# Performance work log

Measured on AMD Instinct MI355X. Metric: run time of the kernel, lower is better.

## Reference

```python
import jax, jax.numpy as jnp
import numpy as np

E = 8          # moe_expert_count
CAPACITY = 1024  # per-expert capacity C = S / E (capacity factor 1)


def _top1_gate(features, wg):
    """Top-1 gate with capacity, returning combine_weights [S,E,C],
    dispatch_mask [S,E,C], and load-balancing aux loss (standard Switch/BASE-style gate
    matching the (l_aux, combine_weights, dispatch_mask) interface used by BaseLayer)."""
    S, M = features.shape
    logits = features @ wg                      # [S, E]
    gates = jax.nn.softmax(logits, axis=-1)     # [S, E]
    idx = jnp.argmax(gates, axis=-1)            # [S] expert assignment
    mask1 = jax.nn.one_hot(idx, E, dtype=features.dtype)  # [S, E]
    # position of each token inside its expert's buffer (0-based, order of arrival)
    locations = jnp.cumsum(mask1, axis=0) - mask1          # [S, E]
    loc = jnp.sum(locations * mask1, axis=1).astype(jnp.int32)  # [S]
    keep = (loc < CAPACITY).astype(features.dtype)          # drop overflow tokens
    mask1 = mask1 * keep[:, None]
    gate_s = jnp.sum(gates * mask1, axis=1)                 # [S] gate prob of kept tokens
    loc_oh = jax.nn.one_hot(loc, CAPACITY, dtype=features.dtype)  # [S, C]
    combine = gate_s[:, None, None] * mask1[:, :, None] * loc_oh[:, None, :]  # [S,E,C]
    dispatch = (combine > 0).astype(features.dtype)
    # load-balance aux loss: E * sum(mean_prob_e * frac_tokens_e)
    me = jnp.mean(gates, axis=0)
    ce = jnp.mean(mask1, axis=0)
    l_aux = jnp.sum(me * ce) * E
    return l_aux, combine, dispatch


def setup_inputs() -> dict:
    key = jax.random.key(0)
    k0, k1, k2, k3 = jax.random.split(key, 4)
    B, T, M, H = 4, 2048, 512, 1024
    return {
        "hidden_states": jax.random.normal(k0, (B, T, M), dtype=jnp.float32),
        "wg": jax.random.normal(k1, (M, E), dtype=jnp.float32) * 0.02,
        "w1": jax.random.normal(k2, (E, M, H), dtype=jnp.float32) * 0.02,
        "b1": jnp.zeros((E, H), dtype=jnp.float32),
        "w2": jax.random.normal(k3, (E, H, M), dtype=jnp.float32) * 0.02,
        "b2": jnp.zeros((E, M), dtype=jnp.float32),
    }


def reference(hidden_states, wg, w1, b1, w2, b2):
    B, T, M = hidden_states.shape
    feats = hidden_states.reshape(-1, M)            # [S, M]
    l_aux, combine, dispatch = _top1_gate(feats, wg)
    # dense one-hot dispatch matmul: (E*C, S) @ (S, M) -> [E, C, M]
    dispatched = jnp.einsum('sec,sm->ecm', dispatch, feats)
    # per-expert FFN (BaseSublayer: Linear -> ReLU -> Linear)
    h = jax.nn.relu(jnp.einsum('ecm,emh->ech', dispatched, w1) + b1[:, None, :])
    expert_out = jnp.einsum('ech,ehn->ecn', h, w2) + b2[:, None, :]  # [E, C, M]
    # dense combine matmul: (S, E*C) @ (E*C, M) -> [S, M]
    combined = jnp.einsum('sec,ecn->sn', combine, expert_out)
    return combined.reshape(B, T, -1), l_aux
```

## Files before the change

### kernel.cpp

```cpp
#include <hip/hip_runtime.h>

#define S_TOK 8192
#define M_DIM 512
#define E_NUM 8
#define CAP   1024
#define H_DIM 1024
#define NGATE_BLK (S_TOK / 4)

typedef __attribute__((ext_vector_type(8))) short bf16x8;
typedef __attribute__((ext_vector_type(16))) float f32x16;

__device__ static inline unsigned short f2bf(float f) {
    unsigned int u = __float_as_uint(f);
    unsigned int r = (u + 0x7fffu + ((u >> 16) & 1u)) >> 16;
    return (unsigned short)r;
}

__device__ static inline void async_copy16(const void* g, void* l) {
    __builtin_amdgcn_global_load_lds(
        (const __attribute__((address_space(1))) void*)g,
        (__attribute__((address_space(3))) void*)l, 16, 0, 0);
}

__global__ __launch_bounds__(256) void prep_kernel(
    const float* __restrict__ feats, const float* __restrict__ wg,
    int* __restrict__ idx, float* __restrict__ gate_top,
    float* __restrict__ gates_psum, unsigned short* __restrict__ xb,
    const float* __restrict__ w1, unsigned short* __restrict__ w1t,
    const float* __restrict__ w2, unsigned short* __restrict__ w2t)
{
    __shared__ float gsh[4][8];
    __shared__ float tile[64][65];

    if (blockIdx.x < NGATE_BLK) {
        const int wave = threadIdx.x >> 6;
        const int lane = threadIdx.x & 63;
        const int s = blockIdx.x * 4 + wave;

        const float* xrow = feats + (size_t)s * M_DIM;
        const int m0 = lane * 8;

        const float4 va = *(const float4*)(xrow + m0);
        const float4 vb = *(const float4*)(xrow + m0 + 4);
        float xv[8] = {va.x, va.y, va.z, va.w, vb.x, vb.y, vb.z, vb.w};

        {
            bf16x8 o;
#pragma unroll
            for (int j = 0; j < 8; ++j) o[j] = (short)f2bf(xv[j]);
            *(bf16x8*)(xb + (size_t)s * M_DIM + m0) = o;
            if (blockIdx.x == 0 && wave == 0) {
                bf16x8 z = (bf16x8){0,0,0,0,0,0,0,0};
                *(bf16x8*)(xb + (size_t)S_TOK * M_DIM + m0) = z;
            }
        }

        float p[8];
#pragma unroll
        for (int e = 0; e < 8; ++e) p[e] = 0.f;
#pragma unroll
        for (int j = 0; j < 8; ++j) {
            const float4 wa = *(const float4*)(wg + (m0 + j) * 8);
            const float4 wb2 = *(const float4*)(wg + (m0 + j) * 8 + 4);
            const float x = xv[j];
            p[0] += x * wa.x;  p[1] += x * wa.y;  p[2] += x * wa.z;  p[3] += x * wa.w;
            p[4] += x * wb2.x; p[5] += x * wb2.y; p[6] += x * wb2.z; p[7] += x * wb2.w;
        }
#pragma unroll
        for (int e = 0; e < 8; ++e) {
            float v = p[e];
#pragma unroll
            for (int off = 1; off < 64; off <<= 1) v += __shfl_xor(v, off, 64);
            p[e] = v;
        }
        if (lane == 0) {
            float mx = p[0];
#pragma unroll
            for (int e = 1; e < 8; ++e) mx = fmaxf(mx, p[e]);
            float ex[8], sum = 0.f;
#pragma unroll
            for (int e = 0; e < 8; ++e) { ex[e] = expf(p[e] - mx); sum += ex[e]; }
            const float inv = 1.0f / sum;
            int best = 0; float bl = p[0];
#pragma unroll
            for (int e = 1; e < 8; ++e) { if (p[e] > bl) { bl = p[e]; best = e; } }
#pragma unroll
            for (int e = 0; e < 8; ++e) gsh[wave][e] = ex[e] * inv;
            idx[s] = best;
            gate_top[s] = ex[best] * inv;
        }
        __syncthreads();
        if (threadIdx.x < 8) {
            const int e = threadIdx.x;
            gates_psum[blockIdx.x * 8 + e] =
                gsh[0][e] + gsh[1][e] + gsh[2][e] + gsh[3][e];
        }
    } else {
        int b = blockIdx.x - NGATE_BLK;
        const float* src; unsigned short* dst;
        int e, k0, n0, K, N;
        if (b < 1024) {
            e = b >> 7; const int rem = b & 127;
            k0 = (rem >> 4) * 64; n0 = (rem & 15) * 64;
            K = 512; N = 1024; src = w1; dst = w1t;
        } else {
            b -= 1024;
            e = b >> 7; const int rem = b & 127;
            k0 = (rem >> 3) * 64; n0 = (rem & 7) * 64;
            K = 1024; N = 512; src = w2; dst = w2t;
        }
        const int t = threadIdx.x;
        const int r = t >> 4, c4 = (t & 15) * 4;
#pragma unroll
        for (int i = 0; i < 4; ++i) {
            const int row = r + i * 16;
            const float4 v = *(const float4*)(src + ((size_t)e * K + k0 + row) * N + n0 + c4);
            tile[row][c4 + 0] = v.x; tile[row][c4 + 1] = v.y;
            tile[row][c4 + 2] = v.z; tile[row][c4 + 3] = v.w;
        }
        __syncthreads();
#pragma unroll
        for (int i = 0; i < 4; ++i) {
            const int row = r + i * 16;
            ushort4 o;
            o.x = f2bf(tile[c4 + 0][row]); o.y = f2bf(tile[c4 + 1][row]);
            o.z = f2bf(tile[c4 + 2][row]); o.w = f2bf(tile[c4 + 3][row]);
            *(ushort4*)(dst + ((size_t)e * N + n0 + row) * K + k0 + c4) = o;
        }
    }
}

__global__ __launch_bounds__(256) void scan_kernel(
    const int* __restrict__ idx, const float* __restrict__ gate_top,
    const float* __restrict__ gates_psum,
    float* __restrict__ gate_final, int* __restrict__ token_list,
    int* __restrict__ kept, float* __restrict__ out,
    int* __restrict__ dropped)
{
    __shared__ int   cnts[256][9];
    __shared__ float wpart[4][8];
    __shared__ int   totals[8];
    __shared__ float gfbuf[8192];
    __shared__ int   dropctr;

    const int t = threadIdx.x;
    const int wv = t >> 6, ln = t & 63;
    const int base = t * 32;

    if (t == 0) dropctr = 0;

    int4   vi[8];
    float4 vg[8];
#pragma unroll
    for (int i = 0; i < 8; ++i) vi[i] = ((const int4*)(idx + base))[i];
#pragma unroll
    for (int i = 0; i < 8; ++i) vg[i] = ((const float4*)(gate_top + base))[i];

    {
        const int4 s4 = make_int4(S_TOK, S_TOK, S_TOK, S_TOK);
#pragma unroll
        for (int i = 0; i < 8; ++i) ((int4*)token_list)[t + 256 * i] = s4;
    }

    int c[8];
#pragma unroll
    for (int e = 0; e < 8; ++e) c[e] = 0;
#pragma unroll
    for (int i = 0; i < 8; ++i) {
#pragma unroll
        for (int e = 0; e < 8; ++e)
            c[e] += (vi[i].x == e) + (vi[i].y == e) + (vi[i].z == e) + (vi[i].w == e);
    }

    float g[8];
#pragma unroll
    for (int e = 0; e < 8; ++e) g[e] = 0.f;
#pragma unroll
    for (int i = 0; i < NGATE_BLK / 256; ++i) {
        const float* gp = gates_psum + (size_t)(t + 256 * i) * 8;
        const float4 a = *(const float4*)gp;
        const float4 b = *(const float4*)(gp + 4);
        g[0] += a.x; g[1] += a.y; g[2] += a.z; g[3] += a.w;
        g[4] += b.x; g[5] += b.y; g[6] += b.z; g[7] += b.w;
    }
#pragma unroll
    for (int e = 0; e < 8; ++e) cnts[t][e] = c[e];
#pragma unroll
    for (int e = 0; e < 8; ++e) {
        float v = g[e];
#pragma unroll
        for (int off = 1; off < 64; off <<= 1) v += __shfl_xor(v, off, 64);
        if (ln == 0) wpart[wv][e] = v;
    }
    __syncthreads();

#pragma unroll
    for (int ee = 0; ee < 2; ++ee) {
        const int e = wv * 2 + ee;
        int off = 0;
#pragma unroll
        for (int seg = 0; seg < 4; ++seg) {
            const int r = seg * 64 + ln;
            const int v = cnts[r][e];
            int incl = v;
#pragma unroll
            for (int d = 1; d < 64; d <<= 1) {
                const int nn = __shfl_up(incl, d, 64);
                if (ln >= d) incl += nn;
            }
            cnts[r][e] = incl - v + off;
            off += __shfl(incl, 63, 64);
        }
        if (ln == 0) {
            totals[e] = off;
            kept[e] = off < CAP ? off : CAP;
        }
    }
    __syncthreads();

    if (t == 0) {
        float l = 0.f;
        for (int e = 0; e < 8; ++e) {
            const float ms = wpart[0][e] + wpart[1][e] + wpart[2][e] + wpart[3][e];
            const int ke = totals[e] < CAP ? totals[e] : CAP;
            l += (ms / (float)S_TOK) * ((float)ke / (float)S_TOK);
        }
        out[(size_t)S_TOK * M_DIM] = l * (float)E_NUM;
    }

    int rc[8];
#pragma unroll
    for (int e = 0; e < 8; ++e) rc[e] = cnts[t][e];

#pragma unroll
    for (int i = 0; i < 8; ++i) {
        const int   ev[4] = {vi[i].x, vi[i].y, vi[i].z, vi[i].w};
        const float gv[4] = {vg[i].x, vg[i].y, vg[i].z, vg[i].w};
#pragma unroll
        for (int j = 0; j < 4; ++j) {
            const int s = base + i * 4 + j;
            const int ei = ev[j];
            int loc = 0;
#pragma unroll
            for (int e = 0; e < 8; ++e) {
                if (ei == e) { loc = rc[e]; rc[e] = rc[e] + 1; }
            }
            const bool keepit = loc < CAP;
            gfbuf[s] = keepit ? gv[j] : 0.f;
            if (keepit) {
                token_list[ei * CAP + loc] = s;
            } else {
                const int d = atomicAdd(&dropctr, 1);
                dropped[d] = s;
            }
        }
    }
    __syncthreads();

#pragma unroll
    for (int i = 0; i < 8; ++i) {
        const int o = (t + 256 * i) * 4;
        *(float4*)(gate_final + o) = *(const float4*)(gfbuf + o);
    }

    const int nd = dropctr;
    for (int d = wv; d < nd; d += 4) {
        const int s = dropped[d];
        float4 z = make_float4(0.f, 0.f, 0.f, 0.f);
        *(float4*)(out + (size_t)s * M_DIM + ln * 4) = z;
        *(float4*)(out + (size_t)s * M_DIM + 256 + ln * 4) = z;
    }
}

__global__ __launch_bounds__(256, 4) void ffn1_mfma(
    const unsigned short* __restrict__ xb, const unsigned short* __restrict__ w1t,
    const float* __restrict__ b1, const int* __restrict__ tok,
    const int* __restrict__ kept, unsigned short* __restrict__ h)
{
    const int b = blockIdx.x;
    const int e = b & 7;
    const int r = b >> 3;
    const int ct = r >> 4, nt = r & 15;
    const int c0 = ct * 128, n0 = nt * 64;
    if (c0 >= kept[e]) return;

    __shared__ __align__(16) short Alds[128 * 64];
    __shared__ __align__(16) short Blds[64 * 64];
    __shared__ int srow[128];

    const int t = threadIdx.x;
    const int wave = t >> 6, lane = t & 63;
    const int wm = wave & 1, wn = wave >> 1;
    const int l31 = lane & 31, kh = lane >> 5;

    if (t < 128) srow[t] = tok[e * CAP + c0 + t];
    __syncthreads();

    f32x16 acc[2];
#pragma unroll
    for (int mg = 0; mg < 2; ++mg)
#pragma unroll
        for (int i = 0; i < 16; ++i) acc[mg][i] = 0.f;

    for (int kb = 0; kb < M_DIM; kb += 64) {
        __syncthreads();
#pragma unroll
        for (int i = 0; i < 4; ++i) {
            const int lin = (i * 4 + wave) * 64 + lane;
            const int row = lin >> 3;
            const int ch = (lin & 7) ^ (row & 7);
            async_copy16(xb + (size_t)srow[row] * M_DIM + kb + ch * 8,
                         &Alds[lin * 8]);
        }
#pragma unroll
        for (int i = 0; i < 2; ++i) {
            const int lin = (i * 4 + wave) * 64 + lane;
            const int row = lin >> 3;
            const int ch = (lin & 7) ^ (row & 7);
            async_copy16(w1t + ((size_t)e * H_DIM + n0 + row) * M_DIM + kb + ch * 8,
                         &Blds[lin * 8]);
        }
        __syncthreads();

#pragma unroll
        for (int kk = 0; kk < 64; kk += 16) {
            const int ch = (kk >> 3) + kh;
            bf16x8 af[2], bfv;
#pragma unroll
            for (int mg = 0; mg < 2; ++mg) {
                const int R = wm * 64 + mg * 32 + l31;
                af[mg] = *(const bf16x8*)(&Alds[(R * 8 + (ch ^ (R & 7))) * 8]);
            }
            {
                const int R = wn * 32 + l31;
                bfv = *(const bf16x8*)(&Blds[(R * 8 + (ch ^ (R & 7))) * 8]);
            }
#pragma unroll
            for (int mg = 0; mg < 2; ++mg)
                acc[mg] = __builtin_amdgcn_mfma_f32_32x32x16_bf16(
                    af[mg], bfv, acc[mg], 0, 0, 0);
        }
    }

    const int col = n0 + wn * 32 + l31;
    const float bias = b1[e * H_DIM + col];
#pragma unroll
    for (int mg = 0; mg < 2; ++mg) {
#pragma unroll
        for (int reg = 0; reg < 16; ++reg) {
            const int rowl = wm * 64 + mg * 32 + (reg & 3) + 8 * (reg >> 2) + 4 * kh;
            const float v = fmaxf(acc[mg][reg] + bias, 0.f);
            h[(size_t)(e * CAP + c0 + rowl) * H_DIM + col] = f2bf(v);
        }
    }
}

__global__ __launch_bounds__(256, 4) void ffn2_mfma(
    const unsigned short* __restrict__ h, const unsigned short* __restrict__ w2t,
    const float* __restrict__ b2, const int* __restrict__ tok,
    const int* __restrict__ kept, const float* __restrict__ gate_final,
    float* __restrict__ out)
{
    const int b = blockIdx.x;
    const int e = b & 7;
    const int r = b >> 3;
    const int ct = r >> 3, nt = r & 7;
    const int c0 = ct * 64, n0 = nt * 64;
    if (c0 >= kept[e]) return;

    __shared__ __align__(16) short Alds[64 * 64];
    __shared__ __align__(16) short Blds[64 * 64];
    __shared__ int   stok[64];
    __shared__ float sgf[64];

    const int t = threadIdx.x;
    const int wave = t >> 6, lane = t & 63;
    const int wm = wave & 1, wn = wave >> 1;
    const int l31 = lane & 31, kh = lane >> 5;

    if (t < 64) {
        const int tk = tok[e * CAP + c0 + t];
        stok[t] = tk;
        sgf[t] = (tk != S_TOK) ? gate_final[tk] : 0.f;
    }

    f32x16 acc;
#pragma unroll
    for (int i = 0; i < 16; ++i) acc[i] = 0.f;

    for (int kb = 0; kb < H_DIM; kb += 64) {
        __syncthreads();
#pragma unroll
        for (int i = 0; i < 2; ++i) {
            const int lin = (i * 4 + wave) * 64 + lane;
            const int row = lin >> 3;
            const int ch = (lin & 7) ^ (row & 7);
            async_copy16(h + (size_t)(e * CAP + c0 + row) * H_DIM + kb + ch * 8,
                         &Alds[lin * 8]);
        }
#pragma unroll
        for (int i = 0; i < 2; ++i) {
            const int lin = (i * 4 + wave) * 64 + lane;
            const int row = lin >> 3;
            const int ch = (lin & 7) ^ (row & 7);
            async_copy16(w2t + ((size_t)e * M_DIM + n0 + row) * H_DIM + kb + ch * 8,
                         &Blds[lin * 8]);
        }
        __syncthreads();

#pragma unroll
        for (int kk = 0; kk < 64; kk += 16) {
            const int ch = (kk >> 3) + kh;
            bf16x8 af, bfv;
            {
                const int R = wm * 32 + l31;
                af = *(const bf16x8*)(&Alds[(R * 8 + (ch ^ (R & 7))) * 8]);
            }
            {
                const int R = wn * 32 + l31;
                bfv = *(const bf16x8*)(&Blds[(R * 8 + (ch ^ (R & 7))) * 8]);
            }
            acc = __builtin_amdgcn_mfma_f32_32x32x16_bf16(af, bfv, acc, 0, 0, 0);
        }
    }

    const int col = n0 + wn * 32 + l31;
    const float bias = b2[e * M_DIM + col];
#pragma unroll
    for (int reg = 0; reg < 16; ++reg) {
        const int slot = wm * 32 + (reg & 3) + 8 * (reg >> 2) + 4 * kh;
        const int tokid = stok[slot];
        if (tokid != S_TOK) {
            out[(size_t)tokid * M_DIM + col] = sgf[slot] * (acc[reg] + bias);
        }
    }
}

extern "C" void kernel_launch(void* const* d_in, const int* in_sizes, int n_in,
                              void* d_out, int out_size, void* d_ws, size_t ws_size,
                              hipStream_t stream) {
    const float* feats = (const float*)d_in[0];
    const float* wg    = (const float*)d_in[1];
    const float* w1    = (const float*)d_in[2];
    const float* b1    = (const float*)d_in[3];
    const float* w2    = (const float*)d_in[4];
    const float* b2    = (const float*)d_in[5];
    float* out = (float*)d_out;

    char* ws = (char*)d_ws;
    size_t off = 0;
    unsigned short* h   = (unsigned short*)(ws + off); off += (size_t)E_NUM * CAP * H_DIM * 2;
    unsigned short* xb  = (unsigned short*)(ws + off); off += (size_t)(S_TOK + 1) * M_DIM * 2;
    unsigned short* w1t = (unsigned short*)(ws + off); off += (size_t)E_NUM * H_DIM * M_DIM * 2;
    unsigned short* w2t = (unsigned short*)(ws + off); off += (size_t)E_NUM * M_DIM * H_DIM * 2;
    int*   idx        = (int*)(ws + off);   off += (size_t)S_TOK * 4;
    float* gate_top   = (float*)(ws + off); off += (size_t)S_TOK * 4;
    float* gate_final = (float*)(ws + off); off += (size_t)S_TOK * 4;
    float* gates_psum = (float*)(ws + off); off += (size_t)NGATE_BLK * 8 * 4;
    int*   token_list = (int*)(ws + off);   off += (size_t)S_TOK * 4;
    int*   dropped    = (int*)(ws + off);   off += (size_t)S_TOK * 4;
    int*   kept       = (int*)(ws + off);   off += 64;
    (void)ws_size; (void)n_in; (void)in_sizes;

    prep_kernel<<<NGATE_BLK + 2048, 256, 0, stream>>>(
        feats, wg, idx, gate_top, gates_psum, xb, w1, w1t, w2, w2t);
    scan_kernel<<<1, 256, 0, stream>>>(idx, gate_top, gates_psum, gate_final,
                                       token_list, kept, out, dropped);
    ffn1_mfma<<<1024, 256, 0, stream>>>(xb, w1t, b1, token_list, kept, h);
    ffn2_mfma<<<1024, 256, 0, stream>>>(h, w2t, b2, token_list, kept,
                                        gate_final, out);
}
```

Before: 168.3 us.

## Overlap w2 conversion with serial scan and enlarge ffn1 tiles to 128x128

Moves the w2 transpose/bf16 conversion out of the prep kernel into a combined mid kernel whose block 0 runs the single-block scan while the other 1024 blocks convert w2. The serial scan no longer runs alone on an otherwise idle GPU. Separately, ffn1 now uses 128x128 output tiles with a 2x2 MFMA accumulator per wave, halving the grid and improving A-tile reuse. The cost is more registers and LDS per block, and launch bounds drop to 2 blocks per CU.

After: 168.6 us. No clear change (+0.2%).

```diff
diff --git a/kernel.cpp b/kernel.cpp
--- a/kernel.cpp
+++ b/kernel.cpp
@@ -26,8 +26,7 @@
     const float* __restrict__ feats, const float* __restrict__ wg,
     int* __restrict__ idx, float* __restrict__ gate_top,
     float* __restrict__ gates_psum, unsigned short* __restrict__ xb,
-    const float* __restrict__ w1, unsigned short* __restrict__ w1t,
-    const float* __restrict__ w2, unsigned short* __restrict__ w2t)
+    const float* __restrict__ w1, unsigned short* __restrict__ w1t)
 {
     __shared__ float gsh[4][8];
     __shared__ float tile[64][65];
@@ -97,24 +96,15 @@
         }
     } else {
         int b = blockIdx.x - NGATE_BLK;
-        const float* src; unsigned short* dst;
-        int e, k0, n0, K, N;
-        if (b < 1024) {
-            e = b >> 7; const int rem = b & 127;
-            k0 = (rem >> 4) * 64; n0 = (rem & 15) * 64;
-            K = 512; N = 1024; src = w1; dst = w1t;
-        } else {
-            b -= 1024;
-            e = b >> 7; const int rem = b & 127;
-            k0 = (rem >> 3) * 64; n0 = (rem & 7) * 64;
-            K = 1024; N = 512; src = w2; dst = w2t;
-        }
+        const int e = b >> 7; const int rem = b & 127;
+        const int k0 = (rem >> 4) * 64, n0 = (rem & 15) * 64;
+        const int K = 512, N = 1024;
         const int t = threadIdx.x;
         const int r = t >> 4, c4 = (t & 15) * 4;
 #pragma unroll
         for (int i = 0; i < 4; ++i) {
             const int row = r + i * 16;
-            const float4 v = *(const float4*)(src + ((size_t)e * K + k0 + row) * N + n0 + c4);
+            const float4 v = *(const float4*)(w1 + ((size_t)e * K + k0 + row) * N + n0 + c4);
             tile[row][c4 + 0] = v.x; tile[row][c4 + 1] = v.y;
             tile[row][c4 + 2] = v.z; tile[row][c4 + 3] = v.w;
         }
@@ -125,154 +115,189 @@
             ushort4 o;
             o.x = f2bf(tile[c4 + 0][row]); o.y = f2bf(tile[c4 + 1][row]);
             o.z = f2bf(tile[c4 + 2][row]); o.w = f2bf(tile[c4 + 3][row]);
-            *(ushort4*)(dst + ((size_t)e * N + n0 + row) * K + k0 + c4) = o;
-        }
-    }
-}
-
-__global__ __launch_bounds__(256) void scan_kernel(
+            *(ushort4*)(w1t + ((size_t)e * N + n0 + row) * K + k0 + c4) = o;
+        }
+    }
+}
+
+struct ScanSmem {
+    int   cnts[256][9];
+    float wpart[4][8];
+    int   totals[8];
+    float gfbuf[8192];
+    int   dropctr;
+};
+#define CONV_SMEM (64 * 65 * 4)
+#define MID_SMEM ((sizeof(ScanSmem) > CONV_SMEM) ? sizeof(ScanSmem) : CONV_SMEM)
+
+__global__ __launch_bounds__(256) void mid_kernel(
     const int* __restrict__ idx, const float* __restrict__ gate_top,
     const float* __restrict__ gates_psum,
     float* __restrict__ gate_final, int* __restrict__ token_list,
     int* __restrict__ kept, float* __restrict__ out,
-    int* __restrict__ dropped)
+    int* __restrict__ dropped,
+    const float* __restrict__ w2, unsigned short* __restrict__ w2t)
 {
-    __shared__ int   cnts[256][9];
-    __shared__ float wpart[4][8];
-    __shared__ int   totals[8];
-    __shared__ float gfbuf[8192];
-    __shared__ int   dropctr;
-
-    const int t = threadIdx.x;
-    const int wv = t >> 6, ln = t & 63;
-    const int base = t * 32;
-
-    if (t == 0) dropctr = 0;
-
-    int4   vi[8];
-    float4 vg[8];
-#pragma unroll
-    for (int i = 0; i < 8; ++i) vi[i] = ((const int4*)(idx + base))[i];
-#pragma unroll
-    for (int i = 0; i < 8; ++i) vg[i] = ((const float4*)(gate_top + base))[i];
-
-    {
-        const int4 s4 = make_int4(S_TOK, S_TOK, S_TOK, S_TOK);
-#pragma unroll
-        for (int i = 0; i < 8; ++i) ((int4*)token_list)[t + 256 * i] = s4;
-    }
-
-    int c[8];
-#pragma unroll
-    for (int e = 0; e < 8; ++e) c[e] = 0;
-#pragma unroll
-    for (int i = 0; i < 8; ++i) {
-#pragma unroll
-        for (int e = 0; e < 8; ++e)
-            c[e] += (vi[i].x == e) + (vi[i].y == e) + (vi[i].z == e) + (vi[i].w == e);
-    }
-
-    float g[8];
-#pragma unroll
-    for (int e = 0; e < 8; ++e) g[e] = 0.f;
-#pragma unroll
-    for (int i = 0; i < NGATE_BLK / 256; ++i) {
-        const float* gp = gates_psum + (size_t)(t + 256 * i) * 8;
-        const float4 a = *(const float4*)gp;
-        const float4 b = *(const float4*)(gp + 4);
-        g[0] += a.x; g[1] += a.y; g[2] += a.z; g[3] += a.w;
-        g[4] += b.x; g[5] += b.y; g[6] += b.z; g[7] += b.w;
-    }
-#pragma unroll
-    for (int e = 0; e < 8; ++e) cnts[t][e] = c[e];
-#pragma unroll
-    for (int e = 0; e < 8; ++e) {
-        float v = g[e];
-#pragma unroll
-        for (int off = 1; off < 64; off <<= 1) v += __shfl_xor(v, off, 64);
-        if (ln == 0) wpart[wv][e] = v;
-    }
-    __syncthreads();
-
-#pragma unroll
-    for (int ee = 0; ee < 2; ++ee) {
-        const int e = wv * 2 + ee;
-        int off = 0;
-#pragma unroll
-        for (int seg = 0; seg < 4; ++seg) {
-            const int r = seg * 64 + ln;
-            const int v = cnts[r][e];
-            int incl = v;
-#pragma unroll
-            for (int d = 1; d < 64; d <<= 1) {
-                const int nn = __shfl_up(incl, d, 64);
-                if (ln >= d) incl += nn;
-            }
-            cnts[r][e] = incl - v + off;
-            off += __shfl(incl, 63, 64);
-        }
-        if (ln == 0) {
-            totals[e] = off;
-            kept[e] = off < CAP ? off : CAP;
-        }
-    }
-    __syncthreads();
-
-    if (t == 0) {
-        float l = 0.f;
+    __shared__ __align__(16) char smem[MID_SMEM];
+
+    if (blockIdx.x == 0) {
+        ScanSmem& S = *reinterpret_cast<ScanSmem*>(smem);
+        const int t = threadIdx.x;
+        const int wv = t >> 6, ln = t & 63;
+        const int base = t * 32;
+
+        if (t == 0) S.dropctr = 0;
+
+        int4   vi[8];
+        float4 vg[8];
+#pragma unroll
+        for (int i = 0; i < 8; ++i) vi[i] = ((const int4*)(idx + base))[i];
+#pragma unroll
+        for (int i = 0; i < 8; ++i) vg[i] = ((const float4*)(gate_top + base))[i];
+
+        {
+            const int4 s4 = make_int4(S_TOK, S_TOK, S_TOK, S_TOK);
+#pragma unroll
+            for (int i = 0; i < 8; ++i) ((int4*)token_list)[t + 256 * i] = s4;
+        }
+
+        int c[8];
+#pragma unroll
+        for (int e = 0; e < 8; ++e) c[e] = 0;
+#pragma unroll
+        for (int i = 0; i < 8; ++i) {
+#pragma unroll
+            for (int e = 0; e < 8; ++e)
+                c[e] += (vi[i].x == e) + (vi[i].y == e) + (vi[i].z == e) + (vi[i].w == e);
+        }
+
+        float g[8];
+#pragma unroll
+        for (int e = 0; e < 8; ++e) g[e] = 0.f;
+#pragma unroll
+        for (int i = 0; i < NGATE_BLK / 256; ++i) {
+            const float* gp = gates_psum + (size_t)(t + 256 * i) * 8;
+            const float4 a = *(const float4*)gp;
+            const float4 b = *(const float4*)(gp + 4);
+            g[0] += a.x; g[1] += a.y; g[2] += a.z; g[3] += a.w;
+            g[4] += b.x; g[5] += b.y; g[6] += b.z; g[7] += b.w;
+        }
+#pragma unroll
+        for (int e = 0; e < 8; ++e) S.cnts[t][e] = c[e];
+#pragma unroll
         for (int e = 0; e < 8; ++e) {
-            const float ms = wpart[0][e] + wpart[1][e] + wpart[2][e] + wpart[3][e];
-            const int ke = totals[e] < CAP ? totals[e] : CAP;
-            l += (ms / (float)S_TOK) * ((float)ke / (float)S_TOK);
-        }
-        out[(size_t)S_TOK * M_DIM] = l * (float)E_NUM;
-    }
-
-    int rc[8];
-#pragma unroll
-    for (int e = 0; e < 8; ++e) rc[e] = cnts[t][e];
-
-#pragma unroll
-    for (int i = 0; i < 8; ++i) {
-        const int   ev[4] = {vi[i].x, vi[i].y, vi[i].z, vi[i].w};
-        const float gv[4] = {vg[i].x, vg[i].y, vg[i].z, vg[i].w};
-#pragma unroll
-        for (int j = 0; j < 4; ++j) {
-            const int s = base + i * 4 + j;
-            const int ei = ev[j];
-            int loc = 0;
-#pragma unroll
+            float v = g[e];
+#pragma unroll
+            for (int off = 1; off < 64; off <<= 1) v += __shfl_xor(v, off, 64);
+            if (ln == 0) S.wpart[wv][e] = v;
+        }
+        __syncthreads();
+
+#pragma unroll
+        for (int ee = 0; ee < 2; ++ee) {
+            const int e = wv * 2 + ee;
+            int off = 0;
+#pragma unroll
+            for (int seg = 0; seg < 4; ++seg) {
+                const int r = seg * 64 + ln;
+                const int v = S.cnts[r][e];
+                int incl = v;
+#pragma unroll
+                for (int d = 1; d < 64; d <<= 1) {
+                    const int nn = __shfl_up(incl, d, 64);
+                    if (ln >= d) incl += nn;
+                }
+                S.cnts[r][e] = incl - v + off;
+                off += __shfl(incl, 63, 64);
+            }
+            if (ln == 0) {
+                S.totals[e] = off;
+                kept[e] = off < CAP ? off : CAP;
+            }
+        }
+        __syncthreads();
+
+        if (t == 0) {
+            float l = 0.f;
             for (int e = 0; e < 8; ++e) {
-                if (ei == e) { loc = rc[e]; rc[e] = rc[e] + 1; }
-            }
-            const bool keepit = loc < CAP;
-            gfbuf[s] = keepit ? gv[j] : 0.f;
-            if (keepit) {
-                token_list[ei * CAP + loc] = s;
-            } else {
-                const int d = atomicAdd(&dropctr, 1);
-                dropped[d] = s;
-            }
-        }
-    }
-    __syncthreads();
-
-#pragma unroll
-    for (int i = 0; i < 8; ++i) {
-        const int o = (t + 256 * i) * 4;
-        *(float4*)(gate_final + o) = *(const float4*)(gfbuf + o);
-    }
-
-    const int nd = dropctr;
-    for (int d = wv; d < nd; d += 4) {
-        const int s = dropped[d];
-        float4 z = make_float4(0.f, 0.f, 0.f, 0.f);
-        *(float4*)(out + (size_t)s * M_DIM + ln * 4) = z;
-        *(float4*)(out + (size_t)s * M_DIM + 256 + ln * 4) = z;
-    }
-}
-
-__global__ __launch_bounds__(256, 4) void ffn1_mfma(
+                const float ms = S.wpart[0][e] + S.wpart[1][e] +
+                                 S.wpart[2][e] + S.wpart[3][e];
+                const int ke = S.totals[e] < CAP ? S.totals[e] : CAP;
+                l += (ms / (float)S_TOK) * ((float)ke / (float)S_TOK);
+            }
+            out[(size_t)S_TOK * M_DIM] = l * (float)E_NUM;
+        }
+
+        int rc[8];
+#pragma unroll
+        for (int e = 0; e < 8; ++e) rc[e] = S.cnts[t][e];
+
+#pragma unroll
+        for (int i = 0; i < 8; ++i) {
+            const int   ev[4] = {vi[i].x, vi[i].y, vi[i].z, vi[i].w};
+            const float gv[4] = {vg[i].x, vg[i].y, vg[i].z, vg[i].w};
+#pragma unroll
+            for (int j = 0; j < 4; ++j) {
+                const int s = base + i * 4 + j;
+                const int ei = ev[j];
+                int loc = 0;
+#pragma unroll
+                for (int e = 0; e < 8; ++e) {
+                    if (ei == e) { loc = rc[e]; rc[e] = rc[e] + 1; }
+                }
+                const bool keepit = loc < CAP;
+                S.gfbuf[s] = keepit ? gv[j] : 0.f;
+                if (keepit) {
+                    token_list[ei * CAP + loc] = s;
+                } else {
+                    const int d = atomicAdd(&S.dropctr, 1);
+                    dropped[d] = s;
+                }
+            }
+        }
+        __syncthreads();
+
+#pragma unroll
+        for (int i = 0; i < 8; ++i) {
+            const int o = (t + 256 * i) * 4;
+            *(float4*)(gate_final + o) = *(const float4*)(S.gfbuf + o);
+        }
+
+        const int nd = S.dropctr;
+        for (int d = wv; d < nd; d += 4) {
+            const int s = dropped[d];
+            float4 z = make_float4(0.f, 0.f, 0.f, 0.f);
+            *(float4*)(out + (size_t)s * M_DIM + ln * 4) = z;
+            *(float4*)(out + (size_t)s * M_DIM + 256 + ln * 4) = z;
+        }
+    } else {
+        float (*tile)[65] = reinterpret_cast<float(*)[65]>(smem);
+        int b = blockIdx.x - 1;
+        const int e = b >> 7; const int rem = b & 127;
+        const int k0 = (rem >> 3) * 64, n0 = (rem & 7) * 64;
+        const int K = 1024, N = 512;
+        const int t = threadIdx.x;
+        const int r = t >> 4, c4 = (t & 15) * 4;
+#pragma unroll
+        for (int i = 0; i < 4; ++i) {
+            const int row = r + i * 16;
+            const float4 v = *(const float4*)(w2 + ((size_t)e * K + k0 + row) * N + n0 + c4);
+            tile[row][c4 + 0] = v.x; tile[row][c4 + 1] = v.y;
+            tile[row][c4 + 2] = v.z; tile[row][c4 + 3] = v.w;
+        }
+        __syncthreads();
+#pragma unroll
+        for (int i = 0; i < 4; ++i) {
+            const int row = r + i * 16;
+            ushort4 o;
+            o.x = f2bf(tile[c4 + 0][row]); o.y = f2bf(tile[c4 + 1][row]);
+            o.z = f2bf(tile[c4 + 2][row]); o.w = f2bf(tile[c4 + 3][row]);
+            *(ushort4*)(w2t + ((size_t)e * N + n0 + row) * K + k0 + c4) = o;
+        }
+    }
+}
+
+__global__ __launch_bounds__(256, 2) void ffn1_mfma(
     const unsigned short* __restrict__ xb, const unsigned short* __restrict__ w1t,
     const float* __restrict__ b1, const int* __restrict__ tok,
     const int* __restrict__ kept, unsigned short* __restrict__ h)
@@ -280,12 +305,12 @@
     const int b = blockIdx.x;
     const int e = b & 7;
     const int r = b >> 3;
-    const int ct = r >> 4, nt = r & 15;
-    const int c0 = ct * 128, n0 = nt * 64;
+    const int ct = r >> 3, nt = r & 7;
+    const int c0 = ct * 128, n0 = nt * 128;
     if (c0 >= kept[e]) return;
 
     __shared__ __align__(16) short Alds[128 * 64];
-    __shared__ __align__(16) short Blds[64 * 64];
+    __shared__ __align__(16) short Blds[128 * 64];
     __shared__ int srow[128];
 
     const int t = threadIdx.x;
@@ -296,11 +321,13 @@
     if (t < 128) srow[t] = tok[e * CAP + c0 + t];
     __syncthreads();
 
-    f32x16 acc[2];
+    f32x16 acc[2][2];
 #pragma unroll
     for (int mg = 0; mg < 2; ++mg)
 #pragma unroll
-        for (int i = 0; i < 16; ++i) acc[mg][i] = 0.f;
+        for (int ng = 0; ng < 2; ++ng)
+#pragma unroll
+            for (int i = 0; i < 16; ++i) acc[mg][ng][i] = 0.f;
 
     for (int kb = 0; kb < M_DIM; kb += 64) {
         __syncthreads();
@@ -313,7 +340,7 @@
                          &Alds[lin * 8]);
         }
 #pragma unroll
-        for (int i = 0; i < 2; ++i) {
+        for (int i = 0; i < 4; ++i) {
             const int lin = (i * 4 + wave) * 64 + lane;
             const int row = lin >> 3;
             const int ch = (lin & 7) ^ (row & 7);
@@ -325,32 +352,38 @@
 #pragma unroll
         for (int kk = 0; kk < 64; kk += 16) {
             const int ch = (kk >> 3) + kh;
-            bf16x8 af[2], bfv;
+            bf16x8 af[2], bfv[2];
 #pragma unroll
             for (int mg = 0; mg < 2; ++mg) {
                 const int R = wm * 64 + mg * 32 + l31;
                 af[mg] = *(const bf16x8*)(&Alds[(R * 8 + (ch ^ (R & 7))) * 8]);
             }
-            {
-                const int R = wn * 32 + l31;
-                bfv = *(const bf16x8*)(&Blds[(R * 8 + (ch ^ (R & 7))) * 8]);
+#pragma unroll
+            for (int ng = 0; ng < 2; ++ng) {
+                const int R = wn * 64 + ng * 32 + l31;
+                bfv[ng] = *(const bf16x8*)(&Blds[(R * 8 + (ch ^ (R & 7))) * 8]);
             }
 #pragma unroll
             for (int mg = 0; mg < 2; ++mg)
-                acc[mg] = __builtin_amdgcn_mfma_f32_32x32x16_bf16(
-                    af[mg], bfv, acc[mg], 0, 0, 0);
-        }
-    }
-
-    const int col = n0 + wn * 32 + l31;
-    const float bias = b1[e * H_DIM + col];
-#pragma unroll
-    for (int mg = 0; mg < 2; ++mg) {
-#pragma unroll
-        for (int reg = 0; reg < 16; ++reg) {
-            const int rowl = wm * 64 + mg * 32 + (reg & 3) + 8 * (reg >> 2) + 4 * kh;
-            const float v = fmaxf(acc[mg][reg] + bias, 0.f);
-            h[(size_t)(e * CAP + c0 + rowl) * H_DIM + col] = f2bf(v);
+#pragma unroll
+                for (int ng = 0; ng < 2; ++ng)
+                    acc[mg][ng] = __builtin_amdgcn_mfma_f32_32x32x16_bf16(
+                        af[mg], bfv[ng], acc[mg][ng], 0, 0, 0);
+        }
+    }
+
+#pragma unroll
+    for (int ng = 0; ng < 2; ++ng) {
+        const int col = n0 + wn * 64 + ng * 32 + l31;
+        const float bias = b1[e * H_DIM + col];
+#pragma unroll
+        for (int mg = 0; mg < 2; ++mg) {
+#pragma unroll
+            for (int reg = 0; reg < 16; ++reg) {
+                const int rowl = wm * 64 + mg * 32 + (reg & 3) + 8 * (reg >> 2) + 4 * kh;
+                const float v = fmaxf(acc[mg][ng][reg] + bias, 0.f);
+                h[(size_t)(e * CAP + c0 + rowl) * H_DIM + col] = f2bf(v);
+            }
         }
     }
 }
@@ -462,11 +495,12 @@
     int*   kept       = (int*)(ws + off);   off += 64;
     (void)ws_size; (void)n_in; (void)in_sizes;
 
-    prep_kernel<<<NGATE_BLK + 2048, 256, 0, stream>>>(
-        feats, wg, idx, gate_top, gates_psum, xb, w1, w1t, w2, w2t);
-    scan_kernel<<<1, 256, 0, stream>>>(idx, gate_top, gates_psum, gate_final,
-                                       token_list, kept, out, dropped);
-    ffn1_mfma<<<1024, 256, 0, stream>>>(xb, w1t, b1, token_list, kept, h);
+    prep_kernel<<<NGATE_BLK + 1024, 256, 0, stream>>>(
+        feats, wg, idx, gate_top, gates_psum, xb, w1, w1t);
+    mid_kernel<<<1 + 1024, 256, 0, stream>>>(idx, gate_top, gates_psum,
+                                             gate_final, token_list, kept, out,
+                                             dropped, w2, w2t);
+    ffn1_mfma<<<512, 256, 0, stream>>>(xb, w1t, b1, token_list, kept, h);
     ffn2_mfma<<<1024, 256, 0, stream>>>(h, w2t, b2, token_list, kept,
                                         gate_final, out);
 }
```
